# Performance work log

Measured on AMD Instinct MI355X. Metric: run time of the kernel, lower is better.

Reference implementation:

```python
import jax, jax.numpy as jnp
import numpy as np

EPS = 1e-5
DT_RANK = 64
N_STATE = 16


def _rmsnorm(x, w):
    var = jnp.mean(x * x, axis=-1, keepdims=True)
    return x * jax.lax.rsqrt(var + EPS) * w


def _softplus(x, beta=1.0, threshold=20.0):
    return jnp.where(beta * x > threshold, x, (1.0 / beta) * jnp.logaddexp(0.0, beta * x))


def _silu(x):
    return x * jax.nn.sigmoid(x)


def setup_inputs() -> dict:
    key = jax.random.key(0)
    ks = jax.random.split(key, 8)
    B, L, H = 2, 1024, 2048  # hidden_size = expand * d_model = 2048
    s = 0.02
    A = jnp.tile(jnp.arange(1.0, N_STATE + 1.0)[None, :], (H, 1))  # (H, 16)
    return {
        "x": jax.random.normal(ks[0], (B, L, H), jnp.float32),
        "norm_w": jnp.ones((H,), jnp.float32),
        "in_proj_w": jax.random.normal(ks[1], (2 * H, H), jnp.float32) * s,
        "conv_w": jax.random.normal(ks[2], (4, H, H), jnp.float32) * s,  # (K, Cin, Cout) LIO
        "conv_b": jnp.zeros((H,), jnp.float32),
        "x_proj_w": jax.random.normal(ks[3], (DT_RANK + 2 * N_STATE, H), jnp.float32) * s,
        "dt_proj_w": jax.random.normal(ks[4], (H, DT_RANK), jnp.float32) * s,
        "dt_proj_b": jnp.zeros((H,), jnp.float32),
        "A_log": jnp.log(A),
        "D": jnp.ones((H,), jnp.float32),
        "out_proj_w": jax.random.normal(ks[5], (H, H), jnp.float32) * s,
    }


def _scan_combine(left, right):
    aL, xL = left
    aR, xR = right
    return aR * aL, aR * xL + xR


def reference(x, norm_w, in_proj_w, conv_w, conv_b, x_proj_w, dt_proj_w, dt_proj_b, A_log, D, out_proj_w):
    B, L, H = x.shape
    h = _rmsnorm(x, norm_w)
    xz = h @ in_proj_w.T                      # (B, L, 2H)
    xc, z = jnp.split(xz, 2, axis=-1)         # each (B, L, H)
    # causal conv1d: mlx pads k-1 both sides then takes first L -> left pad only
    xc = jax.lax.conv_general_dilated(
        xc, conv_w, window_strides=(1,), padding=[(3, 0)],
        dimension_numbers=("NLC", "LIO", "NLC")) + conv_b
    xc = _silu(xc)
    # SSM
    A = -jnp.exp(A_log)                       # (H, N)
    dBC = xc @ x_proj_w.T                     # (B, L, dt_rank + 2N)
    delta = dBC[..., :DT_RANK]
    Bm = dBC[..., DT_RANK:DT_RANK + N_STATE]  # (B, L, N)
    Cm = dBC[..., DT_RANK + N_STATE:]         # (B, L, N)
    delta = _softplus(delta @ dt_proj_w.T + dt_proj_b)  # (B, L, H)
    deltaA = jnp.exp(delta[..., None] * A)              # (B, L, H, N)
    BX = (delta * xc)[..., None] * Bm[:, :, None, :]    # (B, L, H, N)
    _, hs = jax.lax.associative_scan(_scan_combine, (deltaA, BX), axis=1)
    y = jnp.einsum("blhn,bln->blh", hs, Cm) + D * xc
    out = (y * _silu(z)) @ out_proj_w.T
    return x + out
```

## Files before the change

### kernel.cpp

```cpp
#include <hip/hip_runtime.h>
#include <math.h>

typedef unsigned short u16;
typedef __bf16 bf16x8 __attribute__((ext_vector_type(8)));
typedef float f32x4 __attribute__((ext_vector_type(4)));
typedef unsigned short u16x8 __attribute__((ext_vector_type(8)));
typedef unsigned short u16x4 __attribute__((ext_vector_type(4)));

#define H 2048
#define LSEQ 1024
#define LP (LSEQ+3)
#define CL 32
#define NCH 32

__device__ __forceinline__ float bf2f(u16 u) {
    union { float f; unsigned int i; } x; x.i = ((unsigned int)u) << 16; return x.f;
}
__device__ __forceinline__ u16 f2bf(float f) {
    union { float f; unsigned int i; } x; x.f = f;
    unsigned int r = x.i + 0x7fffu + ((x.i >> 16) & 1u);
    return (u16)(r >> 16);
}

__device__ __forceinline__ void gload_lds16(const void* g, void* l) {
    __builtin_amdgcn_global_load_lds((const __attribute__((address_space(1))) void*)g,
                                     (__attribute__((address_space(3))) void*)l,
                                     16, 0, 0);
}

enum { EPI_XZ = 0, EPI_DELTA = 1, EPI_STORE = 5, EPI_P2 = 6 };

template<int EPI, bool APAD>
__launch_bounds__(512, 2)
__global__ void gemmA(const u16* __restrict__ A, const u16* __restrict__ B,
                      int lda, int ldb, long aZoff, long bZoff, int iters,
                      void* __restrict__ out0, void* __restrict__ out1,
                      void* __restrict__ out2, const float* __restrict__ aux) {
    __shared__ u16 As[3][128 * 32];
    __shared__ u16 Bs[3][256 * 32];
    const int m0 = blockIdx.x * 128;
    const int n0 = blockIdx.y * 256;
    const int z  = blockIdx.z;
    const int tid = threadIdx.x;
    const int lane = tid & 63;
    const int w = tid >> 6;
    const int wr = w >> 2;
    const int wc = w & 3;

    long abase;
    if (APAD) {
        int b = m0 >> 10, l0 = m0 & 1023;
        abase = (long)(b * LP + l0) * lda;
    } else {
        abase = (long)m0 * lda;
    }
    const u16* Ag = A + abase + (long)z * aZoff;
    const u16* Bg = B + (long)n0 * ldb + (long)z * bZoff;

    const int sw8 = ((((lane & 15) >> 1) & 3) ^ (lane >> 4)) * 8;

    f32x4 acc[4][4];
#pragma unroll
    for (int i = 0; i < 4; i++)
#pragma unroll
        for (int j = 0; j < 4; j++) acc[i][j] = (f32x4){0.f, 0.f, 0.f, 0.f};

#define STG(s, bi)                                                                \
    {                                                                             \
        const int k0_ = (s) * 32;                                                 \
        {                                                                         \
            const int rA_ = tid >> 2;                                             \
            const int sgA_ = ((tid & 3) ^ ((rA_ >> 1) & 3)) * 8;                  \
            gload_lds16(Ag + (long)rA_ * lda + k0_ + sgA_, &As[bi][tid * 8]);     \
        }                                                                         \
        _Pragma("unroll")                                                         \
        for (int l_ = 0; l_ < 2; l_++) {                                          \
            const int idx_ = l_ * 512 + tid;                                      \
            const int rB_ = idx_ >> 2;                                            \
            const int sgB_ = ((idx_ & 3) ^ ((rB_ >> 1) & 3)) * 8;                 \
            gload_lds16(Bg + (long)rB_ * ldb + k0_ + sgB_, &Bs[bi][idx_ * 8]);    \
        }                                                                         \
    }

    STG(0, 0);
    if (iters > 1) {
        STG(1, 1);
        asm volatile("s_waitcnt vmcnt(3)" ::: "memory");
    } else {
        asm volatile("s_waitcnt vmcnt(0)" ::: "memory");
    }
    __builtin_amdgcn_s_barrier();
    __builtin_amdgcn_sched_barrier(0);

    int cur = 0;
    for (int t = 0; t < iters; ++t) {
        const int nb = (cur == 2) ? 0 : cur + 1;
        const int sb = (nb == 2) ? 0 : nb + 1;
        if (t + 2 < iters) STG(t + 2, sb);

        bf16x8 af[4], bfr[4];
#pragma unroll
        for (int i = 0; i < 4; i++) {
            const int row = wr * 64 + i * 16 + (lane & 15);
            af[i] = *(const bf16x8*)&As[cur][row * 32 + sw8];
        }
#pragma unroll
        for (int j = 0; j < 4; j++) {
            const int row = wc * 64 + j * 16 + (lane & 15);
            bfr[j] = *(const bf16x8*)&Bs[cur][row * 32 + sw8];
        }
        __builtin_amdgcn_s_setprio(1);
#pragma unroll
        for (int i = 0; i < 4; i++)
#pragma unroll
            for (int j = 0; j < 4; j++)
                acc[i][j] = __builtin_amdgcn_mfma_f32_16x16x32_bf16(af[i], bfr[j], acc[i][j], 0, 0, 0);
        __builtin_amdgcn_s_setprio(0);

        if (t < iters - 1) {
            if (t + 2 < iters) asm volatile("s_waitcnt vmcnt(3)" ::: "memory");
            else               asm volatile("s_waitcnt vmcnt(0)" ::: "memory");
            __builtin_amdgcn_s_barrier();
            __builtin_amdgcn_sched_barrier(0);
        }
        cur = nb;
    }
#undef STG

#pragma unroll
    for (int i = 0; i < 4; i++) {
#pragma unroll
        for (int j = 0; j < 4; j++) {
#pragma unroll
            for (int r = 0; r < 4; r++) {
                const int m = m0 + wr * 64 + i * 16 + ((lane >> 4) << 2) + r;
                const int n = n0 + wc * 64 + j * 16 + (lane & 15);
                float v = acc[i][j][r];
                if constexpr (EPI == EPI_XZ) {
                    const int b = m >> 10, l = m & 1023;
                    if (n < H) ((u16*)out0)[((long)(b * LP + l + 3)) * H + n] = f2bf(v);
                    else       ((u16*)out1)[(long)m * H + (n - H)] = f2bf(v);
                } else {
                    if (z == 0) {
                        ((float*)out0)[(long)m * H + n] = v;
                    } else {
                        float* p = (m < 1024) ? (float*)out1 : (float*)out2;
                        p[(long)(m & 1023) * H + n] = v;
                    }
                }
            }
        }
    }
}

template<int EPI, bool APAD>
__launch_bounds__(256)
__global__ void gemm_bt(const u16* __restrict__ A, const u16* __restrict__ B,
                        int K, long aZoff, long bZoff, int itersZ, int ldc,
                        void* __restrict__ out0, void* __restrict__ out1,
                        const float* __restrict__ bias) {
    __shared__ u16 As[128 * 32];
    __shared__ u16 Bs[128 * 32];
    const int m0 = blockIdx.x * 128;
    const int n0 = blockIdx.y * 128;
    const int z  = blockIdx.z;
    const int tid = threadIdx.x;
    const int lane = tid & 63;
    const int w = tid >> 6;
    const int wr = w >> 1, wc = w & 1;

    long abase = (long)m0 * K;
    const u16* Ag = A + abase + (long)z * aZoff;
    const u16* Bg = B + (long)n0 * K + (long)z * bZoff;

    const int sw8 = ((((lane & 15) >> 1) & 3) ^ (lane >> 4)) * 8;

    f32x4 acc[4][4];
#pragma unroll
    for (int i = 0; i < 4; i++)
#pragma unroll
        for (int j = 0; j < 4; j++) acc[i][j] = (f32x4){0.f, 0.f, 0.f, 0.f};

    for (int kt = 0; kt < itersZ; ++kt) {
        const int k0 = kt * 32;
        __syncthreads();
#pragma unroll
        for (int j = 0; j < 2; j++) {
            const int idx = j * 256 + tid;
            const int r = idx >> 2;
            const int segG = ((idx & 3) ^ ((r >> 1) & 3)) * 8;
            gload_lds16(Ag + (long)r * K + k0 + segG, &As[idx * 8]);
            gload_lds16(Bg + (long)r * K + k0 + segG, &Bs[idx * 8]);
        }
        __syncthreads();
        bf16x8 af[4], bfr[4];
#pragma unroll
        for (int i = 0; i < 4; i++) {
            const int row = wr * 64 + i * 16 + (lane & 15);
            af[i] = *(const bf16x8*)&As[row * 32 + sw8];
        }
#pragma unroll
        for (int j = 0; j < 4; j++) {
            const int row = wc * 64 + j * 16 + (lane & 15);
            bfr[j] = *(const bf16x8*)&Bs[row * 32 + sw8];
        }
#pragma unroll
        for (int i = 0; i < 4; i++)
#pragma unroll
            for (int j = 0; j < 4; j++)
                acc[i][j] = __builtin_amdgcn_mfma_f32_16x16x32_bf16(af[i], bfr[j], acc[i][j], 0, 0, 0);
    }

#pragma unroll
    for (int i = 0; i < 4; i++) {
#pragma unroll
        for (int j = 0; j < 4; j++) {
#pragma unroll
            for (int r = 0; r < 4; r++) {
                const int m = m0 + wr * 64 + i * 16 + ((lane >> 4) << 2) + r;
                const int n = n0 + wc * 64 + j * 16 + (lane & 15);
                float v = acc[i][j][r];
                if constexpr (EPI == EPI_DELTA) {
                    v += bias[n];
                    v = (v > 20.f) ? v : log1pf(expf(v));
                    ((float*)out0)[(long)m * H + n] = v;
                }
            }
        }
    }
}

template<int EPI, bool APAD>
__launch_bounds__(256)
__global__ void gemm128d(const u16* __restrict__ A, const u16* __restrict__ B,
                         int lda, int ldb, int iters,
                         long aZoff, long bZoff, long oZoff, int ldo,
                         void* __restrict__ out0, void* __restrict__ out1,
                         const float* __restrict__ aux) {
    __shared__ u16 As[6][128 * 32];
    __shared__ u16 Bs[6][128 * 32];
    const int m0 = blockIdx.y * 128;
    const int n0 = blockIdx.x * 128;
    const int z  = blockIdx.z;
    const int tid = threadIdx.x;
    const int lane = tid & 63;
    const int w = tid >> 6;
    const int wr = w >> 1, wc = w & 1;

    long abase = (long)m0 * lda;
    const u16* Ag = A + abase + (long)z * aZoff;
    const u16* Bg = B + (long)n0 * ldb + (long)z * bZoff;

    const int sw8 = ((((lane & 15) >> 1) & 3) ^ (lane >> 4)) * 8;

    f32x4 acc[4][4];
#pragma unroll
    for (int i = 0; i < 4; i++)
#pragma unroll
        for (int j = 0; j < 4; j++) acc[i][j] = (f32x4){0.f, 0.f, 0.f, 0.f};

#define STG(s, bi)                                                                \
    {                                                                             \
        const int k0_ = (s) * 32;                                                 \
        _Pragma("unroll")                                                         \
        for (int l_ = 0; l_ < 2; l_++) {                                          \
            const int idx_ = l_ * 256 + tid;                                      \
            const int r_ = idx_ >> 2;                                             \
            const int segG_ = ((idx_ & 3) ^ ((r_ >> 1) & 3)) * 8;                 \
            gload_lds16(Ag + (long)r_ * lda + k0_ + segG_, &As[bi][idx_ * 8]);    \
            gload_lds16(Bg + (long)r_ * ldb + k0_ + segG_, &Bs[bi][idx_ * 8]);    \
        }                                                                         \
    }

    STG(0, 0);
    if (iters > 1) STG(1, 1);
    if (iters > 2) STG(2, 2);
    if (iters > 3) STG(3, 3);
    if (iters > 4) STG(4, 4);
    {
        const int pre = iters < 5 ? iters : 5;
        if      (pre == 5) asm volatile("s_waitcnt vmcnt(16)" ::: "memory");
        else if (pre == 4) asm volatile("s_waitcnt vmcnt(12)" ::: "memory");
        else if (pre == 3) asm volatile("s_waitcnt vmcnt(8)" ::: "memory");
        else if (pre == 2) asm volatile("s_waitcnt vmcnt(4)" ::: "memory");
        else               asm volatile("s_waitcnt vmcnt(0)" ::: "memory");
    }
    __builtin_amdgcn_s_barrier();
    __builtin_amdgcn_sched_barrier(0);

    int cur = 0;
    for (int t = 0; t < iters; ++t) {
        const int sb = cur ? cur - 1 : 5;
        if (t + 5 < iters) STG(t + 5, sb);

        bf16x8 af[4], bfr[4];
#pragma unroll
        for (int i = 0; i < 4; i++) {
            const int row = wr * 64 + i * 16 + (lane & 15);
            af[i] = *(const bf16x8*)&As[cur][row * 32 + sw8];
        }
#pragma unroll
        for (int j = 0; j < 4; j++) {
            const int row = wc * 64 + j * 16 + (lane & 15);
            bfr[j] = *(const bf16x8*)&Bs[cur][row * 32 + sw8];
        }
        __builtin_amdgcn_s_setprio(1);
#pragma unroll
        for (int i = 0; i < 4; i++)
#pragma unroll
            for (int j = 0; j < 4; j++)
                acc[i][j] = __builtin_amdgcn_mfma_f32_16x16x32_bf16(af[i], bfr[j], acc[i][j], 0, 0, 0);
        __builtin_amdgcn_s_setprio(0);

        if (t < iters - 1) {
            const int lastst = (t + 5 < iters - 1) ? t + 5 : iters - 1;
            const int ahead = lastst - (t + 1);
            if      (ahead >= 4) asm volatile("s_waitcnt vmcnt(16)" ::: "memory");
            else if (ahead == 3) asm volatile("s_waitcnt vmcnt(12)" ::: "memory");
            else if (ahead == 2) asm volatile("s_waitcnt vmcnt(8)" ::: "memory");
            else if (ahead == 1) asm volatile("s_waitcnt vmcnt(4)" ::: "memory");
            else                 asm volatile("s_waitcnt vmcnt(0)" ::: "memory");
            __builtin_amdgcn_s_barrier();
            __builtin_amdgcn_sched_barrier(0);
        }
        cur = (cur == 5) ? 0 : cur + 1;
    }
#undef STG

#pragma unroll
    for (int i = 0; i < 4; i++) {
#pragma unroll
        for (int j = 0; j < 4; j++) {
#pragma unroll
            for (int r = 0; r < 4; r++) {
                const int m = m0 + wr * 64 + i * 16 + ((lane >> 4) << 2) + r;
                const int n = n0 + wc * 64 + j * 16 + (lane & 15);
                float v = acc[i][j][r];
                if constexpr (EPI == EPI_STORE) {
                    ((float*)out0 + (long)z * oZoff)[(long)m * ldo + n] = v;
                }
            }
        }
    }
}

__global__ void fin_conv2(const float* __restrict__ p0, const float* __restrict__ p1a,
                          const float* __restrict__ p1b, const float* __restrict__ bias,
                          u16* __restrict__ xcc) {
    const long i = ((long)blockIdx.x * 256 + threadIdx.x) * 4;
    f32x4 a = *(const f32x4*)(p0 + i);
    const long half = (long)1024 * 2048;
    const float* p1 = (i < half) ? p1a : p1b;
    const long i1 = (i < half) ? i : i - half;
    f32x4 b = *(const f32x4*)(p1 + i1);
    const int n = (int)(i & 2047);
    f32x4 bv = *(const f32x4*)(bias + n);
    u16x4 o;
#pragma unroll
    for (int j = 0; j < 4; j++) {
        float t = a[j] + b[j] + bv[j];
        o[j] = f2bf(t / (1.f + expf(-t)));
    }
    *(u16x4*)(xcc + i) = o;
}

__global__ void fin_out2(const float* __restrict__ p0, const float* __restrict__ p1a,
                         const float* __restrict__ p1b, const float* __restrict__ x,
                         float* __restrict__ out) {
    const long i = ((long)blockIdx.x * 256 + threadIdx.x) * 4;
    f32x4 a = *(const f32x4*)(p0 + i);
    const long half = (long)1024 * 2048;
    const float* p1 = (i < half) ? p1a : p1b;
    const long i1 = (i < half) ? i : i - half;
    f32x4 b = *(const f32x4*)(p1 + i1);
    f32x4 xv = *(const f32x4*)(x + i);
    f32x4 v;
#pragma unroll
    for (int j = 0; j < 4; j++) v[j] = xv[j] + a[j] + b[j];
    *(f32x4*)(out + i) = v;
}

__global__ void fin_dbc_k(const float* __restrict__ pacc, float* __restrict__ dbc,
                          u16* __restrict__ dbc64) {
    const int i = blockIdx.x * 256 + threadIdx.x;
    const int m = i >> 7, n = i & 127;
    float v = 0.f;
#pragma unroll
    for (int zz = 0; zz < 8; zz++) v += pacc[zz * 262144 + i];
    if (n < 96) dbc[m * 96 + n] = v;
    if (n < 64) dbc64[m * 64 + n] = f2bf(v);
}

__global__ void transpose_w(const float* __restrict__ in, u16* __restrict__ out) {
    __shared__ u16 s[64][72];
    const int tap = blockIdx.z;
    const long base = (long)tap * H * H;
    const int i0 = blockIdx.x * 64, o0 = blockIdx.y * 64;
    const int r = threadIdx.x >> 3;
    const int c = (threadIdx.x & 7) * 8;
#pragma unroll
    for (int rr = r; rr < 64; rr += 32) {
        f32x4 a = *(const f32x4*)&in[base + (long)(i0 + rr) * H + o0 + c];
        f32x4 b = *(const f32x4*)&in[base + (long)(i0 + rr) * H + o0 + c + 4];
#pragma unroll
        for (int j = 0; j < 4; j++) { s[rr][c + j] = f2bf(a[j]); s[rr][c + 4 + j] = f2bf(b[j]); }
    }
    __syncthreads();
#pragma unroll
    for (int rr = r; rr < 64; rr += 32) {
        u16x8 v;
#pragma unroll
        for (int j = 0; j < 8; j++) v[j] = s[c + j][rr];
        *(u16x8*)&out[(long)(o0 + rr) * (4 * H) + (long)tap * H + i0 + c] = v;
    }
}

__global__ void cast_f2b_k(const float* __restrict__ in, u16* __restrict__ out) {
    const long i = ((long)blockIdx.x * 256 + threadIdx.x) * 4;
    f32x4 v = *(const f32x4*)(in + i);
    u16x4 o;
#pragma unroll
    for (int j = 0; j < 4; j++) o[j] = f2bf(v[j]);
    *(u16x4*)(out + i) = o;
}

__global__ void pad_zero_k(u16* __restrict__ xcp) {
    const int i = blockIdx.x * 256 + threadIdx.x;
    const int b = i / (3 * H);
    const int r = i - b * 3 * H;
    xcp[(long)b * LP * H + r] = 0;
}

__global__ void xpw_k(const float* __restrict__ xp, u16* __restrict__ out) {
    const int i = blockIdx.x * 256 + threadIdx.x;
    const int r = i >> 11;
    out[i] = (r < 96) ? f2bf(xp[i]) : (u16)0;
}

__global__ void rmsnorm_k(const float* __restrict__ x, const float* __restrict__ w, u16* __restrict__ h) {
    const long base = (long)blockIdx.x * H;
    const int tid = threadIdx.x;
    f32x4 a = *(const f32x4*)&x[base + tid * 8];
    f32x4 b = *(const f32x4*)&x[base + tid * 8 + 4];
    float f[8];
    float ss = 0.f;
#pragma unroll
    for (int j = 0; j < 4; j++) { f[j] = a[j]; f[4 + j] = b[j]; }
#pragma unroll
    for (int j = 0; j < 8; j++) ss += f[j] * f[j];
#pragma unroll
    for (int m = 32; m > 0; m >>= 1) ss += __shfl_down(ss, m);
    __shared__ float red[4];
    if ((tid & 63) == 0) red[tid >> 6] = ss;
    __syncthreads();
    ss = red[0] + red[1] + red[2] + red[3];
    const float scale = rsqrtf(ss * (1.f / H) + 1e-5f);
    f32x4 wa = *(const f32x4*)&w[tid * 8];
    f32x4 wb = *(const f32x4*)&w[tid * 8 + 4];
    u16x8 o;
#pragma unroll
    for (int j = 0; j < 4; j++) { o[j] = f2bf(f[j] * scale * wa[j]); o[4 + j] = f2bf(f[4 + j] * scale * wb[j]); }
    *(u16x8*)&h[base + tid * 8] = o;
}

__launch_bounds__(256)
__global__ void scan_part1(const float* __restrict__ delta, const u16* __restrict__ xc,
                           const float* __restrict__ dbc, const float* __restrict__ alog,
                           u16* __restrict__ ssum, float* __restrict__ sdl_buf) {
    __shared__ float sB[CL * 16];
    const int tid = threadIdx.x;
    const int bc = blockIdx.x;
    const int b = bc >> 5, c = bc & 31;
    const int h = blockIdx.y * 256 + tid;
    const long tok0 = (long)b * LSEQ + c * CL;
    {
        const int r = tid >> 4, n = tid & 15;
        sB[tid] = dbc[(tok0 + r) * 96 + 64 + n];
        sB[tid + 256] = dbc[(tok0 + r + 16) * 96 + 64 + n];
    }
    __syncthreads();
    float An[16]; bool fast = true;
#pragma unroll
    for (int n = 0; n < 16; n++) {
        An[n] = -expf(alog[h * 16 + n]);
        fast = fast && (fabsf(An[n] + (float)(n + 1)) < 1e-3f * (n + 1));
    }
    float s[16];
#pragma unroll
    for (int n = 0; n < 16; n++) s[n] = 0.f;
    float sdl = 0.f;
    const float* dptr = delta + tok0 * H + h;
    const u16* xptr = xc + tok0 * H + h;
    float dl = dptr[0], xv = bf2f(xptr[0]);
    if (fast) {
        for (int j = 0; j < CL; j++) {
            const long jn = (j < CL - 1) ? (long)(j + 1) * H : (long)j * H;
            const float dl2 = dptr[jn]; const float xv2 = bf2f(xptr[jn]);
            sdl += dl;
            const float e1 = expf(-dl);
            const float u = dl * xv;
            const f32x4* Bv = (const f32x4*)&sB[j * 16];
            float ep = 1.f;
#pragma unroll
            for (int q = 0; q < 4; q++) {
                const f32x4 bb = Bv[q];
#pragma unroll
                for (int k = 0; k < 4; k++) { ep *= e1; s[q*4+k] = ep * s[q*4+k] + u * bb[k]; }
            }
            dl = dl2; xv = xv2;
        }
    } else {
        for (int j = 0; j < CL; j++) {
            const long jn = (j < CL - 1) ? (long)(j + 1) * H : (long)j * H;
            const float dl2 = dptr[jn]; const float xv2 = bf2f(xptr[jn]);
            sdl += dl;
            const float u = dl * xv;
            const f32x4* Bv = (const f32x4*)&sB[j * 16];
#pragma unroll
            for (int q = 0; q < 4; q++) {
                const f32x4 bb = Bv[q];
#pragma unroll
                for (int k = 0; k < 4; k++) { const float e = expf(dl * An[q*4+k]); s[q*4+k] = e * s[q*4+k] + u * bb[k]; }
            }
            dl = dl2; xv = xv2;
        }
    }
    u16x8 o0, o1;
#pragma unroll
    for (int n = 0; n < 8; n++) { o0[n] = f2bf(s[n]); o1[n] = f2bf(s[8 + n]); }
    const long sb = ((long)bc * H + h) * 16;
    *(u16x8*)&ssum[sb] = o0;
    *(u16x8*)&ssum[sb + 8] = o1;
    sdl_buf[(long)bc * H + h] = sdl;
}

__global__ void scan_mid(u16* __restrict__ ssum, const float* __restrict__ sdl_buf,
                         const float* __restrict__ alog) {
    const int tg = blockIdx.x * 256 + threadIdx.x;
    const int b = tg >> 15;
    const int rest = tg & 32767;
    const int h = rest >> 4, n = rest & 15;
    const float An = -expf(alog[h * 16 + n]);
    float S = 0.f;
    for (int c = 0; c < NCH; c++) {
        const long base = (long)(b * NCH + c) * H + h;
        const float a = expf(An * sdl_buf[base]);
        const long si = base * 16 + n;
        const float sloc = bf2f(ssum[si]);
        ssum[si] = f2bf(S);
        S = a * S + sloc;
    }
}

__launch_bounds__(256)
__global__ void scan_part3(const float* __restrict__ delta, const u16* __restrict__ xc,
                           const float* __restrict__ dbc, const float* __restrict__ alog,
                           const float* __restrict__ dvec, const u16* __restrict__ z,
                           const u16* __restrict__ ssum, u16* __restrict__ ybuf) {
    __shared__ float sB[CL * 16];
    __shared__ float sC[CL * 16];
    const int tid = threadIdx.x;
    const int bc = blockIdx.x;
    const int b = bc >> 5, c = bc & 31;
    const int h = blockIdx.y * 256 + tid;
    const long tok0 = (long)b * LSEQ + c * CL;
    {
        const int r = tid >> 4, n = tid & 15;
        sB[tid]       = dbc[(tok0 + r) * 96 + 64 + n];
        sB[tid + 256] = dbc[(tok0 + r + 16) * 96 + 64 + n];
        sC[tid]       = dbc[(tok0 + r) * 96 + 80 + n];
        sC[tid + 256] = dbc[(tok0 + r + 16) * 96 + 80 + n];
    }
    __syncthreads();
    float An[16]; bool fast = true;
#pragma unroll
    for (int n = 0; n < 16; n++) {
        An[n] = -expf(alog[h * 16 + n]);
        fast = fast && (fabsf(An[n] + (float)(n + 1)) < 1e-3f * (n + 1));
    }
    float s[16];
    {
        const long sb = ((long)bc * H + h) * 16;
        u16x8 i0 = *(const u16x8*)&ssum[sb];
        u16x8 i1 = *(const u16x8*)&ssum[sb + 8];
#pragma unroll
        for (int n = 0; n < 8; n++) { s[n] = bf2f(i0[n]); s[8 + n] = bf2f(i1[n]); }
    }
    const float Dh = dvec[h];
    const float* dptr = delta + tok0 * H + h;
    const u16* xptr = xc + tok0 * H + h;
    const u16* zptr = z + tok0 * H + h;
    u16* yptr = ybuf + tok0 * H + h;
    float dl = dptr[0], xv = bf2f(xptr[0]), zf = bf2f(zptr[0]);
    if (fast) {
        for (int j = 0; j < CL; j++) {
            const long jn = (j < CL - 1) ? (long)(j + 1) * H : (long)j * H;
            const float dl2 = dptr[jn]; const float xv2 = bf2f(xptr[jn]); const float zf2 = bf2f(zptr[jn]);
            const float e1 = expf(-dl);
            const float u = dl * xv;
            const f32x4* Bv = (const f32x4*)&sB[j * 16];
            const f32x4* Cv = (const f32x4*)&sC[j * 16];
            float ep = 1.f, y = 0.f;
#pragma unroll
            for (int q = 0; q < 4; q++) {
                const f32x4 bb = Bv[q], cc = Cv[q];
#pragma unroll
                for (int k = 0; k < 4; k++) {
                    ep *= e1;
                    s[q*4+k] = ep * s[q*4+k] + u * bb[k];
                    y += s[q*4+k] * cc[k];
                }
            }
            y += Dh * xv;
            const float g = zf / (1.f + expf(-zf));
            yptr[(long)j * H] = f2bf(y * g);
            dl = dl2; xv = xv2; zf = zf2;
        }
    } else {
        for (int j = 0; j < CL; j++) {
            const long jn = (j < CL - 1) ? (long)(j + 1) * H : (long)j * H;
            const float dl2 = dptr[jn]; const float xv2 = bf2f(xptr[jn]); const float zf2 = bf2f(zptr[jn]);
            const float u = dl * xv;
            const f32x4* Bv = (const f32x4*)&sB[j * 16];
            const f32x4* Cv = (const f32x4*)&sC[j * 16];
            float y = 0.f;
#pragma unroll
            for (int q = 0; q < 4; q++) {
                const f32x4 bb = Bv[q], cc = Cv[q];
#pragma unroll
                for (int k = 0; k < 4; k++) {
                    const float e = expf(dl * An[q*4+k]);
                    s[q*4+k] = e * s[q*4+k] + u * bb[k];
                    y += s[q*4+k] * cc[k];
                }
            }
            y += Dh * xv;
            const float g = zf / (1.f + expf(-zf));
            yptr[(long)j * H] = f2bf(y * g);
            dl = dl2; xv = xv2; zf = zf2;
        }
    }
}

extern "C" void kernel_launch(void* const* d_in, const int* in_sizes, int n_in,
                              void* d_out, int out_size, void* d_ws, size_t ws_size,
                              hipStream_t stream) {
    const float* x       = (const float*)d_in[0];
    const float* norm_w  = (const float*)d_in[1];
    const float* in_proj = (const float*)d_in[2];
    const float* conv_w  = (const float*)d_in[3];
    const float* conv_b  = (const float*)d_in[4];
    const float* x_proj  = (const float*)d_in[5];
    const float* dt_w    = (const float*)d_in[6];
    const float* dt_b    = (const float*)d_in[7];
    const float* a_log   = (const float*)d_in[8];
    const float* Dv      = (const float*)d_in[9];
    const float* out_w   = (const float*)d_in[10];
    float* out = (float*)d_out;

    char* ws = (char*)d_ws;
    u16*   xcp    = (u16*)(ws);
    u16*   hy     = (u16*)(ws + 8413184);
    float* hyF    = (float*)(ws + 8413184);
    u16*   z_buf  = (u16*)(ws + 16801792);
    u16*   wt     = (u16*)(ws + 25190400);
    float* dlt    = (float*)(ws + 25190400);
    u16*   y_buf  = (u16*)(ws + 41967616);
    u16*   ssum   = (u16*)(ws + 50356224);
    u16*   inw    = (u16*)(ws + 58744832);
    float* inwF   = (float*)(ws + 58744832);
    u16*   xpw    = (u16*)(ws + 75522048);
    float* dbc    = (float*)(ws + 76046336);
    u16*   dbc64  = (u16*)(ws + 76832768);
    u16*   dtw    = (u16*)(ws + 77094912);
    float* sdl    = (float*)(ws + 77225984);
    u16*   outw   = (u16*)(ws + 77750272);
    float* outwF  = (float*)(ws + 77750272);
    float* xcpF   = (float*)(ws);

    transpose_w<<<dim3(32, 32, 4), 256, 0, stream>>>(conv_w, wt);
    pad_zero_k<<<48, 256, 0, stream>>>(xcp);
    xpw_k<<<1024, 256, 0, stream>>>(x_proj, xpw);
    cast_f2b_k<<<8192, 256, 0, stream>>>(in_proj, inw);
    cast_f2b_k<<<128, 256, 0, stream>>>(dt_w, dtw);
    rmsnorm_k<<<2048, 256, 0, stream>>>(x, norm_w, hy);

    gemmA<EPI_XZ, false><<<dim3(16, 16, 1), 512, 0, stream>>>(
        hy, inw, 2048, 2048, 0, 0, 64, xcp, z_buf, nullptr, nullptr);

    gemmA<EPI_P2, true><<<dim3(16, 8, 2), 512, 0, stream>>>(
        xcp, wt, 2048, 4 * H, 4096, 4096, 128, inwF, hyF, outwF, nullptr);
    fin_conv2<<<4096, 256, 0, stream>>>(inwF, hyF, outwF, conv_b, (u16*)ws);

    cast_f2b_k<<<4096, 256, 0, stream>>>(out_w, outw);

    gemm128d<EPI_STORE, false><<<dim3(1, 16, 8), 256, 0, stream>>>(
        (u16*)ws, xpw, 2048, 2048, 8, 256, 256, 262144, 128, inwF, nullptr, nullptr);
    fin_dbc_k<<<1024, 256, 0, stream>>>(inwF, dbc, dbc64);

    gemm_bt<EPI_DELTA, false><<<dim3(16, 16, 1), 256, 0, stream>>>(
        dbc64, dtw, 64, 0, 0, 2, 0, dlt, nullptr, dt_b);

    scan_part1<<<dim3(64, 8), 256, 0, stream>>>(dlt, (u16*)ws, dbc, a_log, ssum, sdl);
    scan_mid<<<256, 256, 0, stream>>>(ssum, sdl, a_log);
    scan_part3<<<dim3(64, 8), 256, 0, stream>>>(dlt, (u16*)ws, dbc, a_log, Dv, z_buf, ssum, y_buf);

    gemmA<EPI_P2, false><<<dim3(16, 8, 2), 512, 0, stream>>>(
        y_buf, outw, 2048, 2048, 1024, 1024, 32, inwF, hyF, xcpF, nullptr);
    fin_out2<<<4096, 256, 0, stream>>>(inwF, hyF, xcpF, x, out);
}
```

Baseline: 497.7 us.

## Deepen GEMM LDS pipeline to five stages and remap blocks for L2 locality

Grows the shared-memory ring buffer from three to five stages so global loads run four tiles ahead, with vmcnt waits adjusted to the number of loads in flight. It also remaps the flat block index into panels of eight N-tiles by sixteen M-tiles so concurrently running blocks share A and B tiles in cache. LDS use per block rises to 120KB, which may stop two 512-thread blocks from fitting per CU and lower occupancy. The remap hardcodes 16 M-tiles and assumes the block count divides cleanly into panels, so grids of other shapes could be mapped wrongly.

```diff
diff --git a/kernel.cpp b/kernel.cpp
--- a/kernel.cpp
+++ b/kernel.cpp
@@ -36,11 +36,17 @@
                       int lda, int ldb, long aZoff, long bZoff, int iters,
                       void* __restrict__ out0, void* __restrict__ out1,
                       void* __restrict__ out2, const float* __restrict__ aux) {
-    __shared__ u16 As[3][128 * 32];
-    __shared__ u16 Bs[3][256 * 32];
-    const int m0 = blockIdx.x * 128;
-    const int n0 = blockIdx.y * 256;
-    const int z  = blockIdx.z;
+    __shared__ u16 As[5][128 * 32];
+    __shared__ u16 Bs[5][256 * 32];
+    const int flat = blockIdx.x + gridDim.x * (blockIdx.y + gridDim.y * blockIdx.z);
+    const int xr = flat & 7;
+    const int jj = flat >> 3;
+    const int panel = xr + 8 * (jj >> 4);
+    const int mI = jj & 15;
+    const int m0 = mI * 128;
+    const int yI = panel % gridDim.y;
+    const int z  = panel / gridDim.y;
+    const int n0 = yI * 256;
     const int tid = threadIdx.x;
     const int lane = tid & 63;
     const int w = tid >> 6;
@@ -83,20 +89,23 @@
     }
 
     STG(0, 0);
-    if (iters > 1) {
-        STG(1, 1);
-        asm volatile("s_waitcnt vmcnt(3)" ::: "memory");
-    } else {
-        asm volatile("s_waitcnt vmcnt(0)" ::: "memory");
+    if (iters > 1) STG(1, 1);
+    if (iters > 2) STG(2, 2);
+    if (iters > 3) STG(3, 3);
+    {
+        const int pre = iters < 4 ? iters : 4;
+        if      (pre == 4) asm volatile("s_waitcnt vmcnt(9)" ::: "memory");
+        else if (pre == 3) asm volatile("s_waitcnt vmcnt(6)" ::: "memory");
+        else if (pre == 2) asm volatile("s_waitcnt vmcnt(3)" ::: "memory");
+        else               asm volatile("s_waitcnt vmcnt(0)" ::: "memory");
     }
     __builtin_amdgcn_s_barrier();
     __builtin_amdgcn_sched_barrier(0);
 
     int cur = 0;
     for (int t = 0; t < iters; ++t) {
-        const int nb = (cur == 2) ? 0 : cur + 1;
-        const int sb = (nb == 2) ? 0 : nb + 1;
-        if (t + 2 < iters) STG(t + 2, sb);
+        const int sb = cur ? cur - 1 : 4;
+        if (t + 4 < iters) STG(t + 4, sb);
 
         bf16x8 af[4], bfr[4];
 #pragma unroll
@@ -118,12 +127,16 @@
         __builtin_amdgcn_s_setprio(0);
 
         if (t < iters - 1) {
-            if (t + 2 < iters) asm volatile("s_waitcnt vmcnt(3)" ::: "memory");
-            else               asm volatile("s_waitcnt vmcnt(0)" ::: "memory");
+            const int lastst = (t + 4 < iters - 1) ? t + 4 : iters - 1;
+            const int ahead = lastst - (t + 1);
+            if      (ahead >= 3) asm volatile("s_waitcnt vmcnt(9)" ::: "memory");
+            else if (ahead == 2) asm volatile("s_waitcnt vmcnt(6)" ::: "memory");
+            else if (ahead == 1) asm volatile("s_waitcnt vmcnt(3)" ::: "memory");
+            else                 asm volatile("s_waitcnt vmcnt(0)" ::: "memory");
             __builtin_amdgcn_s_barrier();
             __builtin_amdgcn_sched_barrier(0);
         }
-        cur = nb;
+        cur = (cur == 4) ? 0 : cur + 1;
     }
 #undef STG
 
```

Result: no change. 502.3 us (+0.9%).

## Use intra-block split-K GEMM with BK=64 and fuse residual into out-proj

Applied to the files above, without the earlier changes.

The 128x256 GEMM kernel now has each block cover a BK=64 k-slice. Two groups of four waves each take half of that slice and combine their partial accumulators through LDS at the end, so each wave holds a full 128-row by 64-col tile. The out-projection drops its z-split partial buffers and the separate fin_out2 kernel, and adds the residual x directly in the epilogue. This cuts one launch and the extra fp32 round-trips, but it adds a cross-wave reduction step, raises register use (32 accumulator tiles per wave), and launches half as many blocks for the out-projection.

```diff
diff --git a/kernel.cpp b/kernel.cpp
--- a/kernel.cpp
+++ b/kernel.cpp
@@ -28,24 +28,23 @@
                                      16, 0, 0);
 }
 
-enum { EPI_XZ = 0, EPI_DELTA = 1, EPI_STORE = 5, EPI_P2 = 6 };
+enum { EPI_XZ = 0, EPI_DELTA = 1, EPI_STORE = 5, EPI_P2 = 6, EPI_OUT = 7 };
 
 template<int EPI, bool APAD>
 __launch_bounds__(512, 2)
-__global__ void gemmA(const u16* __restrict__ A, const u16* __restrict__ B,
+__global__ void gemmB(const u16* __restrict__ A, const u16* __restrict__ B,
                       int lda, int ldb, long aZoff, long bZoff, int iters,
                       void* __restrict__ out0, void* __restrict__ out1,
                       void* __restrict__ out2, const float* __restrict__ aux) {
-    __shared__ u16 As[3][128 * 32];
-    __shared__ u16 Bs[3][256 * 32];
+    __shared__ u16 SM[73728];
     const int m0 = blockIdx.x * 128;
     const int n0 = blockIdx.y * 256;
     const int z  = blockIdx.z;
     const int tid = threadIdx.x;
     const int lane = tid & 63;
     const int w = tid >> 6;
-    const int wr = w >> 2;
-    const int wc = w & 3;
+    const int wc2 = w & 3;
+    const int kh = w >> 2;
 
     long abase;
     if (APAD) {
@@ -57,35 +56,37 @@
     const u16* Ag = A + abase + (long)z * aZoff;
     const u16* Bg = B + (long)n0 * ldb + (long)z * bZoff;
 
-    const int sw8 = ((((lane & 15) >> 1) & 3) ^ (lane >> 4)) * 8;
-
-    f32x4 acc[4][4];
-#pragma unroll
-    for (int i = 0; i < 4; i++)
+    const int sw16 = (((kh << 2) + (lane >> 4)) ^ (lane & 7)) * 8;
+
+    f32x4 acc[8][4];
+#pragma unroll
+    for (int i = 0; i < 8; i++)
 #pragma unroll
         for (int j = 0; j < 4; j++) acc[i][j] = (f32x4){0.f, 0.f, 0.f, 0.f};
 
-#define STG(s, bi)                                                                \
-    {                                                                             \
-        const int k0_ = (s) * 32;                                                 \
-        {                                                                         \
-            const int rA_ = tid >> 2;                                             \
-            const int sgA_ = ((tid & 3) ^ ((rA_ >> 1) & 3)) * 8;                  \
-            gload_lds16(Ag + (long)rA_ * lda + k0_ + sgA_, &As[bi][tid * 8]);     \
-        }                                                                         \
-        _Pragma("unroll")                                                         \
-        for (int l_ = 0; l_ < 2; l_++) {                                          \
-            const int idx_ = l_ * 512 + tid;                                      \
-            const int rB_ = idx_ >> 2;                                            \
-            const int sgB_ = ((idx_ & 3) ^ ((rB_ >> 1) & 3)) * 8;                 \
-            gload_lds16(Bg + (long)rB_ * ldb + k0_ + sgB_, &Bs[bi][idx_ * 8]);    \
-        }                                                                         \
+#define STG(s, bi)                                                                   \
+    {                                                                                \
+        const int k0_ = (s) * 64;                                                    \
+        _Pragma("unroll")                                                            \
+        for (int l_ = 0; l_ < 2; l_++) {                                             \
+            const int idx_ = l_ * 512 + tid;                                         \
+            const int r_ = idx_ >> 3;                                                \
+            const int gs_ = ((idx_ & 7) ^ (r_ & 7)) * 8;                             \
+            gload_lds16(Ag + (long)r_ * lda + k0_ + gs_, &SM[(bi) * 8192 + idx_ * 8]); \
+        }                                                                            \
+        _Pragma("unroll")                                                            \
+        for (int l_ = 0; l_ < 4; l_++) {                                             \
+            const int idx_ = l_ * 512 + tid;                                         \
+            const int r_ = idx_ >> 3;                                                \
+            const int gs_ = ((idx_ & 7) ^ (r_ & 7)) * 8;                             \
+            gload_lds16(Bg + (long)r_ * ldb + k0_ + gs_, &SM[24576 + (bi) * 16384 + idx_ * 8]); \
+        }                                                                            \
     }
 
     STG(0, 0);
     if (iters > 1) {
         STG(1, 1);
-        asm volatile("s_waitcnt vmcnt(3)" ::: "memory");
+        asm volatile("s_waitcnt vmcnt(6)" ::: "memory");
     } else {
         asm volatile("s_waitcnt vmcnt(0)" ::: "memory");
     }
@@ -94,58 +95,70 @@
 
     int cur = 0;
     for (int t = 0; t < iters; ++t) {
-        const int nb = (cur == 2) ? 0 : cur + 1;
-        const int sb = (nb == 2) ? 0 : nb + 1;
+        const int sb = cur ? cur - 1 : 2;
         if (t + 2 < iters) STG(t + 2, sb);
 
-        bf16x8 af[4], bfr[4];
-#pragma unroll
-        for (int i = 0; i < 4; i++) {
-            const int row = wr * 64 + i * 16 + (lane & 15);
-            af[i] = *(const bf16x8*)&As[cur][row * 32 + sw8];
-        }
-#pragma unroll
-        for (int j = 0; j < 4; j++) {
-            const int row = wc * 64 + j * 16 + (lane & 15);
-            bfr[j] = *(const bf16x8*)&Bs[cur][row * 32 + sw8];
-        }
+        bf16x8 af[8], bfr[4];
+#pragma unroll
+        for (int i = 0; i < 8; i++)
+            af[i] = *(const bf16x8*)&SM[cur * 8192 + (i * 16 + (lane & 15)) * 64 + sw16];
+#pragma unroll
+        for (int j = 0; j < 4; j++)
+            bfr[j] = *(const bf16x8*)&SM[24576 + cur * 16384 + (wc2 * 64 + j * 16 + (lane & 15)) * 64 + sw16];
         __builtin_amdgcn_s_setprio(1);
 #pragma unroll
-        for (int i = 0; i < 4; i++)
+        for (int i = 0; i < 8; i++)
 #pragma unroll
             for (int j = 0; j < 4; j++)
                 acc[i][j] = __builtin_amdgcn_mfma_f32_16x16x32_bf16(af[i], bfr[j], acc[i][j], 0, 0, 0);
         __builtin_amdgcn_s_setprio(0);
 
         if (t < iters - 1) {
-            if (t + 2 < iters) asm volatile("s_waitcnt vmcnt(3)" ::: "memory");
+            if (t + 2 < iters) asm volatile("s_waitcnt vmcnt(6)" ::: "memory");
             else               asm volatile("s_waitcnt vmcnt(0)" ::: "memory");
             __builtin_amdgcn_s_barrier();
             __builtin_amdgcn_sched_barrier(0);
         }
-        cur = nb;
+        cur = (cur == 2) ? 0 : cur + 1;
     }
 #undef STG
 
-#pragma unroll
-    for (int i = 0; i < 4; i++) {
-#pragma unroll
-        for (int j = 0; j < 4; j++) {
-#pragma unroll
-            for (int r = 0; r < 4; r++) {
-                const int m = m0 + wr * 64 + i * 16 + ((lane >> 4) << 2) + r;
-                const int n = n0 + wc * 64 + j * 16 + (lane & 15);
-                float v = acc[i][j][r];
-                if constexpr (EPI == EPI_XZ) {
-                    const int b = m >> 10, l = m & 1023;
-                    if (n < H) ((u16*)out0)[((long)(b * LP + l + 3)) * H + n] = f2bf(v);
-                    else       ((u16*)out1)[(long)m * H + (n - H)] = f2bf(v);
-                } else {
-                    if (z == 0) {
-                        ((float*)out0)[(long)m * H + n] = v;
+    __syncthreads();
+    float* red = (float*)SM;
+    const int rb = wc2 * 8192;
+    if (kh) {
+#pragma unroll
+        for (int i = 0; i < 8; i++)
+#pragma unroll
+            for (int j = 0; j < 4; j++)
+#pragma unroll
+                for (int r = 0; r < 4; r++)
+                    red[rb + ((i * 4 + j) * 4 + r) * 64 + lane] = acc[i][j][r];
+    }
+    __syncthreads();
+    if (!kh) {
+#pragma unroll
+        for (int i = 0; i < 8; i++) {
+#pragma unroll
+            for (int j = 0; j < 4; j++) {
+#pragma unroll
+                for (int r = 0; r < 4; r++) {
+                    float v = acc[i][j][r] + red[rb + ((i * 4 + j) * 4 + r) * 64 + lane];
+                    const int m = m0 + i * 16 + ((lane >> 4) << 2) + r;
+                    const int n = n0 + wc2 * 64 + j * 16 + (lane & 15);
+                    if constexpr (EPI == EPI_XZ) {
+                        const int b = m >> 10, l = m & 1023;
+                        if (n < H) ((u16*)out0)[((long)(b * LP + l + 3)) * H + n] = f2bf(v);
+                        else       ((u16*)out1)[(long)m * H + (n - H)] = f2bf(v);
+                    } else if constexpr (EPI == EPI_OUT) {
+                        ((float*)out0)[(long)m * H + n] = v + aux[(long)m * H + n];
                     } else {
-                        float* p = (m < 1024) ? (float*)out1 : (float*)out2;
-                        p[(long)(m & 1023) * H + n] = v;
+                        if (z == 0) {
+                            ((float*)out0)[(long)m * H + n] = v;
+                        } else {
+                            float* p = (m < 1024) ? (float*)out1 : (float*)out2;
+                            p[(long)(m & 1023) * H + n] = v;
+                        }
                     }
                 }
             }
@@ -265,7 +278,7 @@
         _Pragma("unroll")                                                         \
         for (int l_ = 0; l_ < 2; l_++) {                                          \
             const int idx_ = l_ * 256 + tid;                                      \
-            const int r_ = idx_ >> 2;                                             \
+            const int r_ = idx_ >> 2;                                            \
             const int segG_ = ((idx_ & 3) ^ ((r_ >> 1) & 3)) * 8;                 \
             gload_lds16(Ag + (long)r_ * lda + k0_ + segG_, &As[bi][idx_ * 8]);    \
             gload_lds16(Bg + (long)r_ * ldb + k0_ + segG_, &Bs[bi][idx_ * 8]);    \
@@ -362,22 +375,6 @@
         o[j] = f2bf(t / (1.f + expf(-t)));
     }
     *(u16x4*)(xcc + i) = o;
-}
-
-__global__ void fin_out2(const float* __restrict__ p0, const float* __restrict__ p1a,
-                         const float* __restrict__ p1b, const float* __restrict__ x,
-                         float* __restrict__ out) {
-    const long i = ((long)blockIdx.x * 256 + threadIdx.x) * 4;
-    f32x4 a = *(const f32x4*)(p0 + i);
-    const long half = (long)1024 * 2048;
-    const float* p1 = (i < half) ? p1a : p1b;
-    const long i1 = (i < half) ? i : i - half;
-    f32x4 b = *(const f32x4*)(p1 + i1);
-    f32x4 xv = *(const f32x4*)(x + i);
-    f32x4 v;
-#pragma unroll
-    for (int j = 0; j < 4; j++) v[j] = xv[j] + a[j] + b[j];
-    *(f32x4*)(out + i) = v;
 }
 
 __global__ void fin_dbc_k(const float* __restrict__ pacc, float* __restrict__ dbc,
@@ -676,7 +673,6 @@
     float* sdl    = (float*)(ws + 77225984);
     u16*   outw   = (u16*)(ws + 77750272);
     float* outwF  = (float*)(ws + 77750272);
-    float* xcpF   = (float*)(ws);
 
     transpose_w<<<dim3(32, 32, 4), 256, 0, stream>>>(conv_w, wt);
     pad_zero_k<<<48, 256, 0, stream>>>(xcp);
@@ -685,11 +681,11 @@
     cast_f2b_k<<<128, 256, 0, stream>>>(dt_w, dtw);
     rmsnorm_k<<<2048, 256, 0, stream>>>(x, norm_w, hy);
 
-    gemmA<EPI_XZ, false><<<dim3(16, 16, 1), 512, 0, stream>>>(
-        hy, inw, 2048, 2048, 0, 0, 64, xcp, z_buf, nullptr, nullptr);
-
-    gemmA<EPI_P2, true><<<dim3(16, 8, 2), 512, 0, stream>>>(
-        xcp, wt, 2048, 4 * H, 4096, 4096, 128, inwF, hyF, outwF, nullptr);
+    gemmB<EPI_XZ, false><<<dim3(16, 16, 1), 512, 0, stream>>>(
+        hy, inw, 2048, 2048, 0, 0, 32, xcp, z_buf, nullptr, nullptr);
+
+    gemmB<EPI_P2, true><<<dim3(16, 8, 2), 512, 0, stream>>>(
+        xcp, wt, 2048, 4 * H, 4096, 4096, 64, inwF, hyF, outwF, nullptr);
     fin_conv2<<<4096, 256, 0, stream>>>(inwF, hyF, outwF, conv_b, (u16*)ws);
 
     cast_f2b_k<<<4096, 256, 0, stream>>>(out_w, outw);
@@ -705,7 +701,6 @@
     scan_mid<<<256, 256, 0, stream>>>(ssum, sdl, a_log);
     scan_part3<<<dim3(64, 8), 256, 0, stream>>>(dlt, (u16*)ws, dbc, a_log, Dv, z_buf, ssum, y_buf);
 
-    gemmA<EPI_P2, false><<<dim3(16, 8, 2), 512, 0, stream>>>(
-        y_buf, outw, 2048, 2048, 1024, 1024, 32, inwF, hyF, xcpF, nullptr);
-    fin_out2<<<4096, 256, 0, stream>>>(inwF, hyF, xcpF, x, out);
-}
+    gemmB<EPI_OUT, false><<<dim3(16, 8, 1), 512, 0, stream>>>(
+        y_buf, outw, 2048, 2048, 0, 0, 32, out, nullptr, nullptr, x);
+}
```

Result: faster. 437.3 us (-12.1%).
